# Kernel tuning notes

Measured on AMD Instinct MI355X. Metric: run time of the kernel, lower is better.

## Reference

```python
import jax, jax.numpy as jnp
import numpy as np

B, T, NB, H = 1024, 128, 13, 128
T_IN = 64  # input_timesteps


def setup_inputs() -> dict:
    key = jax.random.key(0)
    ks = jax.random.split(key, 7)
    s = 1.0 / np.sqrt(H)
    return {
        "x": jax.random.normal(ks[0], (B, T, NB), dtype=jnp.float32),
        "W_ih": jax.random.normal(ks[1], (4 * H, NB), dtype=jnp.float32) * s,
        "W_hh": jax.random.normal(ks[2], (4 * H, H), dtype=jnp.float32) * s,
        "b_ih": jax.random.normal(ks[3], (4 * H,), dtype=jnp.float32) * s,
        "b_hh": jax.random.normal(ks[4], (4 * H,), dtype=jnp.float32) * s,
        "W_out": jax.random.normal(ks[5], (NB, H), dtype=jnp.float32) * s,
        "b_out": jax.random.normal(ks[6], (NB,), dtype=jnp.float32) * s,
    }


def _lstm_cell(x_t, h, c, W_ih, W_hh, b_ih, b_hh):
    # PyTorch nn.LSTM gate order: input, forget, cell(g), output
    gates = x_t @ W_ih.T + h @ W_hh.T + (b_ih + b_hh)  # [B, 4H]
    i, f, g, o = jnp.split(gates, 4, axis=-1)
    i = jax.nn.sigmoid(i)
    f = jax.nn.sigmoid(f)
    g = jnp.tanh(g)
    o = jax.nn.sigmoid(o)
    c_new = f * c + i * g
    h_new = o * jnp.tanh(c_new)
    return h_new, c_new


def reference(x, W_ih, W_hh, b_ih, b_hh, W_out, b_out):
    # forward_train with teacher_forcing=False, gp_enabled=False:
    # 1) teacher-fed LSTM over x[:, :T_IN]
    batch = x.shape[0]
    h0 = jnp.zeros((batch, H), dtype=x.dtype)
    c0 = jnp.zeros((batch, H), dtype=x.dtype)

    def step_teacher(carry, x_t):
        h, c = carry
        h, c = _lstm_cell(x_t, h, c, W_ih, W_hh, b_ih, b_hh)
        y = h @ W_out.T + b_out  # [B, NB]
        return (h, c), y

    (h, c), ys1 = jax.lax.scan(step_teacher, (h0, c0),
                               jnp.swapaxes(x[:, :T_IN], 0, 1))  # ys1: [T_IN, B, NB]

    remaining = T - T_IN - 1

    def step_auto(carry, _):
        h, c, inp = carry
        h, c = _lstm_cell(inp, h, c, W_ih, W_hh, b_ih, b_hh)
        y = h @ W_out.T + b_out
        return (h, c, y), y

    _, ys2 = jax.lax.scan(step_auto, (h, c, x[:, T_IN]), None, length=remaining)

    out = jnp.concatenate([
        x[:, 0:1],
        jnp.swapaxes(ys1, 0, 1),
        jnp.swapaxes(ys2, 0, 1),
    ], axis=1)  # [B, T, NB]
    return out
```

## Files before the change

### kernel.cpp

```cpp
#include <hip/hip_runtime.h>
#include <math.h>

#define BATCH 1024
#define TT    128
#define NBI   13
#define HH    128
#define T_INP 64
#define BB    16
#define NBLK  (BATCH/BB)

typedef _Float16 half8 __attribute__((ext_vector_type(8)));
typedef _Float16 half4 __attribute__((ext_vector_type(4)));
typedef float    f32x4 __attribute__((ext_vector_type(4)));

__device__ __forceinline__ unsigned short f16b(float v) {
    return __builtin_bit_cast(unsigned short, (_Float16)v);
}
__device__ __forceinline__ float rcpf_(float x) { return __builtin_amdgcn_rcpf(x); }
__device__ __forceinline__ float sigmoid_(float v) {
    return rcpf_(1.0f + __expf(-v));
}
__device__ __forceinline__ float tanh_(float v) {
    float e = __expf(2.0f * v);
    return 1.0f - 2.0f * rcpf_(e + 1.0f);
}

#define WS_WHH   0
#define WS_WHAT  131072
#define WS_WIHP  262144
#define WS_WOUT  294912
#define WS_BT    299008
#define WS_BA    301056

__global__ void fold_kernel(const float* __restrict__ W_ih,
                            const float* __restrict__ W_hh,
                            const float* __restrict__ b_ih,
                            const float* __restrict__ b_hh,
                            const float* __restrict__ W_out,
                            const float* __restrict__ b_out,
                            unsigned char* __restrict__ ws)
{
    const int j = blockIdx.x;
    const int k = threadIdx.x;
    unsigned short* whh16  = (unsigned short*)(ws + WS_WHH);
    unsigned short* what16 = (unsigned short*)(ws + WS_WHAT);
    unsigned short* wihp16 = (unsigned short*)(ws + WS_WIHP);
    unsigned short* wout16 = (unsigned short*)(ws + WS_WOUT);
    float* bias_t = (float*)(ws + WS_BT);
    float* bias_a = (float*)(ws + WS_BA);

    float whh = W_hh[j * HH + k];
    float acc = whh;
#pragma unroll
    for (int m = 0; m < NBI; ++m)
        acc += W_ih[j * NBI + m] * W_out[m * HH + k];
    whh16[j * HH + k]  = f16b(whh);
    what16[j * HH + k] = f16b(acc);

    if (k < 32) wihp16[j * 32 + k] = (k < NBI) ? f16b(W_ih[j * NBI + k]) : (unsigned short)0;
    if (k == 0) {
        float bt = b_ih[j] + b_hh[j];
        bias_t[j] = bt;
        float ba = bt;
#pragma unroll
        for (int m = 0; m < NBI; ++m) ba += W_ih[j * NBI + m] * b_out[m];
        bias_a[j] = ba;
    }
    if (j < 16) wout16[j * HH + k] = (j < NBI) ? f16b(W_out[j * HH + k]) : (unsigned short)0;
}

#define MFMA16(A, B, C) __builtin_amdgcn_mfma_f32_16x16x32_f16((A), (B), (C), 0, 0, 0)

__global__ __launch_bounds__(512, 2)
void lstm_main(const float* __restrict__ x,
               const float* __restrict__ b_out,
               const unsigned char* __restrict__ ws,
               float* __restrict__ out)
{
    const int j  = threadIdx.x;
    const int w  = j >> 6;
    const int l  = j & 63;
    const int g  = l >> 4;
    const int cb = l & 15;
    const int bbase = blockIdx.x * BB;

    const unsigned short* whh16  = (const unsigned short*)(ws + WS_WHH);
    const unsigned short* what16 = (const unsigned short*)(ws + WS_WHAT);
    const unsigned short* wihp16 = (const unsigned short*)(ws + WS_WIHP);
    const unsigned short* wout16 = (const unsigned short*)(ws + WS_WOUT);
    const float* btfp = (const float*)(ws + WS_BT);
    const float* bafp = (const float*)(ws + WS_BA);

    __shared__ half8 h_s[2][16][16];
    __shared__ half8 x_s[2][4][16];

    half8 wf[4][4];
    half8 wxf[4];
    half8 wof[4];
    f32x4 binit[4];
#pragma unroll
    for (int gate = 0; gate < 4; ++gate) {
        const int row = 128 * gate + 16 * w + cb;
#pragma unroll
        for (int kk = 0; kk < 4; ++kk)
            wf[gate][kk] = *(const half8*)(whh16 + row * HH + 32 * kk + 8 * g);
        wxf[gate] = *(const half8*)(wihp16 + row * 32 + 8 * g);
#pragma unroll
        for (int r = 0; r < 4; ++r)
            binit[gate][r] = btfp[128 * gate + 16 * w + 4 * g + r];
    }
#pragma unroll
    for (int kk = 0; kk < 4; ++kk)
        wof[kk] = *(const half8*)(wout16 + cb * HH + 32 * kk + 8 * g);

    float bo[4];
#pragma unroll
    for (int r = 0; r < 4; ++r) {
        const int m = 4 * g + r;
        bo[r] = (m < NBI) ? b_out[m] : 0.0f;
    }

    if (j < 256) h_s[0][j >> 4][j & 15] = (half8)(_Float16)0.0f;
    if (j < 128) ((half8*)x_s)[j] = (half8)(_Float16)0.0f;
    __syncthreads();

    int sb = 0, sm = 0;
    const float* xb = x;
    float* ob = out;
    if (j < 208) {
        sb = j / NBI; sm = j - NBI * sb;
        xb = x   + (size_t)(bbase + sb) * TT * NBI;
        ob = out + (size_t)(bbase + sb) * TT * NBI;
        float v = xb[sm];
        ((_Float16*)&x_s[0][sm >> 3][sb])[sm & 7] = (_Float16)v;
        ob[sm] = v;
    }
    __syncthreads();

    f32x4 c = {0.f, 0.f, 0.f, 0.f};
    int cur = 0;

    for (int t = 0; t < TT - 1; ++t) {
        if (t == T_INP + 1) {
#pragma unroll
            for (int gate = 0; gate < 4; ++gate) {
                const int row = 128 * gate + 16 * w + cb;
#pragma unroll
                for (int kk = 0; kk < 4; ++kk)
                    wf[gate][kk] = *(const half8*)(what16 + row * HH + 32 * kk + 8 * g);
#pragma unroll
                for (int r = 0; r < 4; ++r)
                    binit[gate][r] = bafp[128 * gate + 16 * w + 4 * g + r];
            }
        }
        const int nxt = cur ^ 1;

        float xv = 0.0f;
        const bool do_stage = (j < 208) && (t + 1 <= T_INP);
        if (do_stage) xv = xb[(t + 1) * NBI + sm];

        f32x4 acc0 = binit[0], acc1 = binit[1], acc2 = binit[2], acc3 = binit[3];
        if (t <= T_INP) {
            half8 xf = x_s[cur][g][cb];
            acc0 = MFMA16(wxf[0], xf, acc0);
            acc1 = MFMA16(wxf[1], xf, acc1);
            acc2 = MFMA16(wxf[2], xf, acc2);
            acc3 = MFMA16(wxf[3], xf, acc3);
        }
        f32x4 pacc = {0.f, 0.f, 0.f, 0.f};
#pragma unroll
        for (int kk = 0; kk < 4; ++kk) {
            half8 hb = h_s[cur][4 * kk + g][cb];
            acc0 = MFMA16(wf[0][kk], hb, acc0);
            acc1 = MFMA16(wf[1][kk], hb, acc1);
            acc2 = MFMA16(wf[2][kk], hb, acc2);
            acc3 = MFMA16(wf[3][kk], hb, acc3);
            if (w == 0) pacc = MFMA16(wof[kk], hb, pacc);
        }

        half4 h4v;
#pragma unroll
        for (int r = 0; r < 4; ++r) {
            float ig = sigmoid_(acc0[r]);
            float fg = sigmoid_(acc1[r]);
            float gg = tanh_(acc2[r]);
            float og = sigmoid_(acc3[r]);
            float cn = fg * c[r] + ig * gg;
            c[r] = cn;
            h4v[r] = (_Float16)(og * tanh_(cn));
        }
        {
            _Float16* hp = (_Float16*)&h_s[nxt][2 * w + (g >> 1)][cb];
            *(half4*)(hp + 4 * (g & 1)) = h4v;
        }
        if (do_stage)
            ((_Float16*)&x_s[nxt][sm >> 3][sb])[sm & 7] = (_Float16)xv;

        if (w == 0 && t >= 1) {
#pragma unroll
            for (int r = 0; r < 4; ++r) {
                const int m = 4 * g + r;
                if (m < NBI)
                    out[((size_t)(bbase + cb) * TT + t) * NBI + m] = pacc[r] + bo[r];
            }
        }
        __syncthreads();
        cur = nxt;
    }

    if (w == 0) {
        f32x4 pacc = {0.f, 0.f, 0.f, 0.f};
#pragma unroll
        for (int kk = 0; kk < 4; ++kk) {
            half8 hb = h_s[cur][4 * kk + g][cb];
            pacc = MFMA16(wof[kk], hb, pacc);
        }
#pragma unroll
        for (int r = 0; r < 4; ++r) {
            const int m = 4 * g + r;
            if (m < NBI)
                out[((size_t)(bbase + cb) * TT + (TT - 1)) * NBI + m] = pacc[r] + bo[r];
        }
    }
}

extern "C" void kernel_launch(void* const* d_in, const int* in_sizes, int n_in,
                              void* d_out, int out_size, void* d_ws, size_t ws_size,
                              hipStream_t stream)
{
    const float* x     = (const float*)d_in[0];
    const float* W_ih  = (const float*)d_in[1];
    const float* W_hh  = (const float*)d_in[2];
    const float* b_ih  = (const float*)d_in[3];
    const float* b_hh  = (const float*)d_in[4];
    const float* W_out = (const float*)d_in[5];
    const float* b_out = (const float*)d_in[6];
    float* out = (float*)d_out;
    unsigned char* ws = (unsigned char*)d_ws;

    fold_kernel<<<512, HH, 0, stream>>>(W_ih, W_hh, b_ih, b_hh, W_out, b_out, ws);
    lstm_main<<<NBLK, 512, 0, stream>>>(x, b_out, ws, out);
}
```

Measured before the change: 209.3 us.

## Fold gate scaling into weights, split loop phases, prefetch x, use LDS-only barrier

Pre-scales the gate weights and biases by -log2e (2*log2e for the cell gate) so each activation uses a raw exp2 instead of exp with a multiply. Splits the time loop into a teacher phase and an autoregressive phase, which removes per-step branches and the weight reload check. Prefetches x two steps ahead to hide global load latency. Replaces __syncthreads with an LDS-only waitcnt plus s_barrier, so global stores are not waited on at each step. The output projection moves to wave 7 and uses a precomputed pointer. The relaxed barrier depends on global stores never being read back inside the kernel.

Result: faster. 186.4 us (-10.9%).

```diff
diff --git a/kernel.cpp b/kernel.cpp
--- a/kernel.cpp
+++ b/kernel.cpp
@@ -9,6 +9,8 @@
 #define BB    16
 #define NBLK  (BATCH/BB)
 
+#define LOG2E 1.4426950408889634f
+
 typedef _Float16 half8 __attribute__((ext_vector_type(8)));
 typedef _Float16 half4 __attribute__((ext_vector_type(4)));
 typedef float    f32x4 __attribute__((ext_vector_type(4)));
@@ -17,12 +19,18 @@
     return __builtin_bit_cast(unsigned short, (_Float16)v);
 }
 __device__ __forceinline__ float rcpf_(float x) { return __builtin_amdgcn_rcpf(x); }
-__device__ __forceinline__ float sigmoid_(float v) {
-    return rcpf_(1.0f + __expf(-v));
-}
-__device__ __forceinline__ float tanh_(float v) {
-    float e = __expf(2.0f * v);
-    return 1.0f - 2.0f * rcpf_(e + 1.0f);
+
+#if __has_builtin(__builtin_amdgcn_exp2f)
+__device__ __forceinline__ float exp2_(float x) { return __builtin_amdgcn_exp2f(x); }
+#else
+__device__ __forceinline__ float exp2_(float x) { return __expf(x * 0.6931471805599453f); }
+#endif
+
+__device__ __forceinline__ void barrier_lds() {
+    asm volatile("s_waitcnt lgkmcnt(0)" ::: "memory");
+    __builtin_amdgcn_sched_barrier(0);
+    __builtin_amdgcn_s_barrier();
+    __builtin_amdgcn_sched_barrier(0);
 }
 
 #define WS_WHH   0
@@ -49,22 +57,25 @@
     float* bias_t = (float*)(ws + WS_BT);
     float* bias_a = (float*)(ws + WS_BA);
 
+    const int gate = j >> 7;
+    const float sc = (gate == 2) ? (2.0f * LOG2E) : (-LOG2E);
+
     float whh = W_hh[j * HH + k];
     float acc = whh;
 #pragma unroll
     for (int m = 0; m < NBI; ++m)
         acc += W_ih[j * NBI + m] * W_out[m * HH + k];
-    whh16[j * HH + k]  = f16b(whh);
-    what16[j * HH + k] = f16b(acc);
-
-    if (k < 32) wihp16[j * 32 + k] = (k < NBI) ? f16b(W_ih[j * NBI + k]) : (unsigned short)0;
+    whh16[j * HH + k]  = f16b(sc * whh);
+    what16[j * HH + k] = f16b(sc * acc);
+
+    if (k < 32) wihp16[j * 32 + k] = (k < NBI) ? f16b(sc * W_ih[j * NBI + k]) : (unsigned short)0;
     if (k == 0) {
         float bt = b_ih[j] + b_hh[j];
-        bias_t[j] = bt;
+        bias_t[j] = sc * bt;
         float ba = bt;
 #pragma unroll
         for (int m = 0; m < NBI; ++m) ba += W_ih[j * NBI + m] * b_out[m];
-        bias_a[j] = ba;
+        bias_a[j] = sc * ba;
     }
     if (j < 16) wout16[j * HH + k] = (j < NBI) ? f16b(W_out[j * HH + k]) : (unsigned short)0;
 }
@@ -109,6 +120,7 @@
         for (int r = 0; r < 4; ++r)
             binit[gate][r] = btfp[128 * gate + 16 * w + 4 * g + r];
     }
+    const bool projw = (w == 7);
 #pragma unroll
     for (int kk = 0; kk < 4; ++kk)
         wof[kk] = *(const half8*)(wout16 + cb * HH + 32 * kk + 8 * g);
@@ -119,6 +131,7 @@
         const int m = 4 * g + r;
         bo[r] = (m < NBI) ? b_out[m] : 0.0f;
     }
+    float* pob = out + (size_t)(bbase + cb) * TT * NBI + 4 * g;
 
     if (j < 256) h_s[0][j >> 4][j & 15] = (half8)(_Float16)0.0f;
     if (j < 128) ((half8*)x_s)[j] = (half8)(_Float16)0.0f;
@@ -126,41 +139,28 @@
 
     int sb = 0, sm = 0;
     const float* xb = x;
-    float* ob = out;
-    if (j < 208) {
+    const bool do_x = (j < 208);
+    float xv_hold = 0.0f, xv_pref = 0.0f;
+    if (do_x) {
         sb = j / NBI; sm = j - NBI * sb;
-        xb = x   + (size_t)(bbase + sb) * TT * NBI;
-        ob = out + (size_t)(bbase + sb) * TT * NBI;
-        float v = xb[sm];
+        xb = x + (size_t)(bbase + sb) * TT * NBI + sm;
+        float v = xb[0];
         ((_Float16*)&x_s[0][sm >> 3][sb])[sm & 7] = (_Float16)v;
-        ob[sm] = v;
+        out[(size_t)(bbase + sb) * TT * NBI + sm] = v;
+        xv_hold = xb[NBI];
     }
     __syncthreads();
 
     f32x4 c = {0.f, 0.f, 0.f, 0.f};
     int cur = 0;
 
-    for (int t = 0; t < TT - 1; ++t) {
-        if (t == T_INP + 1) {
-#pragma unroll
-            for (int gate = 0; gate < 4; ++gate) {
-                const int row = 128 * gate + 16 * w + cb;
-#pragma unroll
-                for (int kk = 0; kk < 4; ++kk)
-                    wf[gate][kk] = *(const half8*)(what16 + row * HH + 32 * kk + 8 * g);
-#pragma unroll
-                for (int r = 0; r < 4; ++r)
-                    binit[gate][r] = bafp[128 * gate + 16 * w + 4 * g + r];
-            }
-        }
+    for (int t = 0; t <= T_INP; ++t) {
         const int nxt = cur ^ 1;
 
-        float xv = 0.0f;
-        const bool do_stage = (j < 208) && (t + 1 <= T_INP);
-        if (do_stage) xv = xb[(t + 1) * NBI + sm];
+        if (do_x && t + 2 <= T_INP) xv_pref = xb[(t + 2) * NBI];
 
         f32x4 acc0 = binit[0], acc1 = binit[1], acc2 = binit[2], acc3 = binit[3];
-        if (t <= T_INP) {
+        {
             half8 xf = x_s[cur][g][cb];
             acc0 = MFMA16(wxf[0], xf, acc0);
             acc1 = MFMA16(wxf[1], xf, acc1);
@@ -175,40 +175,92 @@
             acc1 = MFMA16(wf[1][kk], hb, acc1);
             acc2 = MFMA16(wf[2][kk], hb, acc2);
             acc3 = MFMA16(wf[3][kk], hb, acc3);
-            if (w == 0) pacc = MFMA16(wof[kk], hb, pacc);
+            if (projw) pacc = MFMA16(wof[kk], hb, pacc);
         }
 
         half4 h4v;
 #pragma unroll
         for (int r = 0; r < 4; ++r) {
-            float ig = sigmoid_(acc0[r]);
-            float fg = sigmoid_(acc1[r]);
-            float gg = tanh_(acc2[r]);
-            float og = sigmoid_(acc3[r]);
+            float ig = rcpf_(1.0f + exp2_(acc0[r]));
+            float fg = rcpf_(1.0f + exp2_(acc1[r]));
+            float eg = exp2_(acc2[r]);
+            float gg = 1.0f - 2.0f * rcpf_(eg + 1.0f);
+            float og = rcpf_(1.0f + exp2_(acc3[r]));
             float cn = fg * c[r] + ig * gg;
             c[r] = cn;
-            h4v[r] = (_Float16)(og * tanh_(cn));
+            float ec = exp2_(cn * 2.8853900817779268f);
+            h4v[r] = (_Float16)(og * (1.0f - 2.0f * rcpf_(ec + 1.0f)));
         }
         {
             _Float16* hp = (_Float16*)&h_s[nxt][2 * w + (g >> 1)][cb];
             *(half4*)(hp + 4 * (g & 1)) = h4v;
         }
-        if (do_stage)
-            ((_Float16*)&x_s[nxt][sm >> 3][sb])[sm & 7] = (_Float16)xv;
-
-        if (w == 0 && t >= 1) {
-#pragma unroll
-            for (int r = 0; r < 4; ++r) {
-                const int m = 4 * g + r;
-                if (m < NBI)
-                    out[((size_t)(bbase + cb) * TT + t) * NBI + m] = pacc[r] + bo[r];
-            }
-        }
-        __syncthreads();
+        if (do_x && t + 1 <= T_INP) {
+            ((_Float16*)&x_s[nxt][sm >> 3][sb])[sm & 7] = (_Float16)xv_hold;
+            xv_hold = xv_pref;
+        }
+        if (projw && t >= 1) {
+#pragma unroll
+            for (int r = 0; r < 4; ++r)
+                if (4 * g + r < NBI) pob[t * NBI + r] = pacc[r] + bo[r];
+        }
+        barrier_lds();
         cur = nxt;
     }
 
-    if (w == 0) {
+#pragma unroll
+    for (int gate = 0; gate < 4; ++gate) {
+        const int row = 128 * gate + 16 * w + cb;
+#pragma unroll
+        for (int kk = 0; kk < 4; ++kk)
+            wf[gate][kk] = *(const half8*)(what16 + row * HH + 32 * kk + 8 * g);
+#pragma unroll
+        for (int r = 0; r < 4; ++r)
+            binit[gate][r] = bafp[128 * gate + 16 * w + 4 * g + r];
+    }
+
+    for (int t = T_INP + 1; t < TT - 1; ++t) {
+        const int nxt = cur ^ 1;
+
+        f32x4 acc0 = binit[0], acc1 = binit[1], acc2 = binit[2], acc3 = binit[3];
+        f32x4 pacc = {0.f, 0.f, 0.f, 0.f};
+#pragma unroll
+        for (int kk = 0; kk < 4; ++kk) {
+            half8 hb = h_s[cur][4 * kk + g][cb];
+            acc0 = MFMA16(wf[0][kk], hb, acc0);
+            acc1 = MFMA16(wf[1][kk], hb, acc1);
+            acc2 = MFMA16(wf[2][kk], hb, acc2);
+            acc3 = MFMA16(wf[3][kk], hb, acc3);
+            if (projw) pacc = MFMA16(wof[kk], hb, pacc);
+        }
+
+        half4 h4v;
+#pragma unroll
+        for (int r = 0; r < 4; ++r) {
+            float ig = rcpf_(1.0f + exp2_(acc0[r]));
+            float fg = rcpf_(1.0f + exp2_(acc1[r]));
+            float eg = exp2_(acc2[r]);
+            float gg = 1.0f - 2.0f * rcpf_(eg + 1.0f);
+            float og = rcpf_(1.0f + exp2_(acc3[r]));
+            float cn = fg * c[r] + ig * gg;
+            c[r] = cn;
+            float ec = exp2_(cn * 2.8853900817779268f);
+            h4v[r] = (_Float16)(og * (1.0f - 2.0f * rcpf_(ec + 1.0f)));
+        }
+        {
+            _Float16* hp = (_Float16*)&h_s[nxt][2 * w + (g >> 1)][cb];
+            *(half4*)(hp + 4 * (g & 1)) = h4v;
+        }
+        if (projw) {
+#pragma unroll
+            for (int r = 0; r < 4; ++r)
+                if (4 * g + r < NBI) pob[t * NBI + r] = pacc[r] + bo[r];
+        }
+        barrier_lds();
+        cur = nxt;
+    }
+
+    if (projw) {
         f32x4 pacc = {0.f, 0.f, 0.f, 0.f};
 #pragma unroll
         for (int kk = 0; kk < 4; ++kk) {
@@ -216,11 +268,8 @@
             pacc = MFMA16(wof[kk], hb, pacc);
         }
 #pragma unroll
-        for (int r = 0; r < 4; ++r) {
-            const int m = 4 * g + r;
-            if (m < NBI)
-                out[((size_t)(bbase + cb) * TT + (TT - 1)) * NBI + m] = pacc[r] + bo[r];
-        }
+        for (int r = 0; r < 4; ++r)
+            if (4 * g + r < NBI) pob[(TT - 1) * NBI + r] = pacc[r] + bo[r];
     }
 }
 
```
